# Performance work log

Measured on AMD Instinct MI355X. Metric: run time of the kernel, lower is better.

The kernel has to match this reference:

```python
import jax, jax.numpy as jnp
import numpy as np

B, R, L, E = 64, 36, 64, 512
LAMBDA_SOFTMAX = 9.0
NORM_EPS = 1e-12   # F.normalize eps
COS_EPS = 1e-8     # F.cosine_similarity eps


def _l2norm(x):
    return x / jnp.maximum(jnp.linalg.norm(x, axis=-1, keepdims=True), NORM_EPS)


def setup_inputs() -> dict:
    key = jax.random.key(0)
    k1, k2, k3 = jax.random.split(key, 3)
    images = jax.random.normal(k1, (B, R, E), dtype=jnp.float32)
    captions = jax.random.normal(k2, (B, L, E), dtype=jnp.float32)
    cap_lens = jax.random.randint(k3, (B,), 1, L + 1, dtype=jnp.int32)
    return {"images": images, "captions": captions, "cap_lens": cap_lens}


def reference(images, captions, cap_lens):
    # images: (B_img, R, E) region features; captions: (B_cap, L, E) token features
    img = _l2norm(images)
    cap = _l2norm(captions)

    # pairwise token-to-region similarity: (cap, img, L, R)
    sim = jnp.einsum('cle,ire->cilr', cap, img)
    # softmax over regions with temperature lambda_softmax.
    # NOTE: the original masks padded TOKEN rows with -inf before this softmax,
    # but those rows' outputs are fully zeroed below, so skipping the -inf fill
    # is mathematically equivalent (and NaN-free).
    attn_w = jax.nn.softmax(LAMBDA_SOFTMAX * sim, axis=-1)
    # attended image vector per (caption, image, token): (cap, img, L, E)
    attn = jnp.einsum('cilr,ire->cile', attn_w, img)

    # cosine similarity over feature dim
    dot = jnp.einsum('cle,cile->cil', cap, attn)
    na = jnp.linalg.norm(cap, axis=-1)[:, None, :]   # (cap, 1, L)
    nb = jnp.linalg.norm(attn, axis=-1)              # (cap, img, L)
    r = dot / jnp.maximum(na * nb, COS_EPS)          # (cap, img, L)

    # zero out padded tokens, then mean over the full padded length L
    valid = (jnp.arange(L)[None, :] < cap_lens[:, None]).astype(r.dtype)  # (cap, L)
    r = r * valid[:, None, :]
    sim_scores = r.mean(axis=-1)  # (cap, img)
    return sim_scores
```

## Files before the change

kernel.cpp:

```cpp
#include <hip/hip_runtime.h>
#include <stdint.h>

#define NCAP 64
#define NIMG 64
#define LTOK 64
#define RREG 36
#define EDIM 512
#define LAM 9.0f
#define SSTR 38

#define IMGT_STRIDE 18432

#define CHUNK_BYTES 34816
#define LDS_BYTES 77824

typedef __attribute__((ext_vector_type(8))) short bf16x8;
typedef __attribute__((ext_vector_type(4))) float f32x4;
typedef __attribute__((ext_vector_type(8))) unsigned short u16x8;

typedef const __attribute__((address_space(1))) void* gas1_t;
typedef __attribute__((address_space(3))) void* las3_t;

__device__ __forceinline__ void gl16(const void* g, void* l) {
  __builtin_amdgcn_global_load_lds((gas1_t)g, (las3_t)l, 16, 0, 0);
}

__device__ __forceinline__ unsigned short f2bf(float f) {
  unsigned int u = __float_as_uint(f);
  u += 0x7FFFu + ((u >> 16) & 1u);
  return (unsigned short)(u >> 16);
}

__global__ __launch_bounds__(256) void k_prep(const float* __restrict__ cap,
                                              const float* __restrict__ img,
                                              unsigned short* __restrict__ capT,
                                              unsigned short* __restrict__ imgT,
                                              float* __restrict__ G2) {
  __shared__ __align__(16) char gfr[49152];
  int tid = threadIdx.x;
  int w = tid >> 6, lane = tid & 63;
  int bid = blockIdx.x;

  if (bid < 64) {
    int i = bid;
    for (int t = tid; t < 1024; t += 256) {
      if ((t & 15) >= 4) {
        u16x8 z = {};
        *(u16x8*)(gfr + 32768 + t * 16) = z;
      }
    }
    int kk = lane >> 2, kg = lane & 3;
#pragma unroll
    for (int t = 0; t < 9; ++t) {
      int r = w + t * 4;
      const float* p = img + ((size_t)i * RREG + r) * EDIM + lane * 8;
      float4 a = *(const float4*)p;
      float4 b = *(const float4*)(p + 4);
      float ss = a.x * a.x + a.y * a.y + a.z * a.z + a.w * a.w +
                 b.x * b.x + b.y * b.y + b.z * b.z + b.w * b.w;
#pragma unroll
      for (int off = 1; off < 64; off <<= 1) ss += __shfl_xor(ss, off);
      float sc = 1.0f / fmaxf(sqrtf(ss), 1e-12f);
      u16x8 o = {f2bf(a.x * sc), f2bf(a.y * sc), f2bf(a.z * sc),
                 f2bf(a.w * sc), f2bf(b.x * sc), f2bf(b.y * sc),
                 f2bf(b.z * sc), f2bf(b.w * sc)};
      *(u16x8*)(gfr + (r >> 4) * 16384 + kk * 1024 +
                ((kg << 4) + (r & 15)) * 16) = o;
    }
    __syncthreads();
    if (w < 3) {
      f32x4 acc3[3];
#pragma unroll
      for (int n = 0; n < 3; ++n) acc3[n] = 0.f;
#pragma unroll
      for (int k2 = 0; k2 < 16; ++k2) {
        bf16x8 av = *(const bf16x8*)(gfr + w * 16384 + k2 * 1024 + lane * 16);
        bf16x8 b0 = *(const bf16x8*)(gfr + 0 * 16384 + k2 * 1024 + lane * 16);
        bf16x8 b1 = *(const bf16x8*)(gfr + 1 * 16384 + k2 * 1024 + lane * 16);
        bf16x8 b2 = *(const bf16x8*)(gfr + 2 * 16384 + k2 * 1024 + lane * 16);
        acc3[0] = __builtin_amdgcn_mfma_f32_16x16x32_bf16(av, b0, acc3[0], 0, 0, 0);
        acc3[1] = __builtin_amdgcn_mfma_f32_16x16x32_bf16(av, b1, acc3[1], 0, 0, 0);
        acc3[2] = __builtin_amdgcn_mfma_f32_16x16x32_bf16(av, b2, acc3[2], 0, 0, 0);
      }
      int rq = lane & 15, kgq = lane >> 4;
#pragma unroll
      for (int n = 0; n < 3; ++n)
#pragma unroll
        for (int j = 0; j < 4; ++j) {
          int R = w * 16 + kgq * 4 + j, C = n * 16 + rq;
          if (R < RREG && C < RREG) {
            float v = acc3[n][j];
            G2[(size_t)i * 1296 + R * 36 + C] = (R == C) ? v : 2.0f * v;
          }
        }
    }
    return;
  }

  int kkw = lane >> 2, kgw = lane & 3;
  int v = (bid - 64) * 4 + w;
  const float* p;
  unsigned short* dst;
  if (v < NCAP * LTOK) {
    int c = v >> 6, row = v & 63;
    int m = row >> 4, rqw = row & 15;
    p = cap + (size_t)v * EDIM + lane * 8;
    dst = capT + (size_t)c * 32768 +
          (size_t)(((m * 16 + kkw) * 64 + kgw * 16 + rqw) * 8);
  } else {
    int vi = v - NCAP * LTOK;
    int i = vi / RREG;
    int r = vi - i * RREG;
    p = img + ((size_t)i * RREG + r) * EDIM + lane * 8;
    if (r < 32) {
      int n = r >> 4, rqw = r & 15;
      dst = imgT + (size_t)i * IMGT_STRIDE +
            (size_t)(((n * 16 + kkw) * 64 + kgw * 16 + rqw) * 8);
    } else {
      int rq2 = r - 32;
      dst = imgT + (size_t)i * IMGT_STRIDE + 16384 +
            (size_t)(kkw * 128 + (kgw * 4 + rq2) * 8);
    }
  }
  float4 a = *(const float4*)p;
  float4 b = *(const float4*)(p + 4);
  float ss = a.x * a.x + a.y * a.y + a.z * a.z + a.w * a.w +
             b.x * b.x + b.y * b.y + b.z * b.z + b.w * b.w;
#pragma unroll
  for (int off = 1; off < 64; off <<= 1) ss += __shfl_xor(ss, off);
  float sc = 1.0f / fmaxf(sqrtf(ss), 1e-12f);
  u16x8 o = {f2bf(a.x * sc), f2bf(a.y * sc), f2bf(a.z * sc), f2bf(a.w * sc),
             f2bf(b.x * sc), f2bf(b.y * sc), f2bf(b.z * sc), f2bf(b.w * sc)};
  *(u16x8*)dst = o;
}

__device__ __forceinline__ void stage_chunk(const unsigned short* capT,
                                            const unsigned short* imgT,
                                            char* buf, int c0, int i0, int ch,
                                            int w, int lane) {
#pragma unroll
  for (int j = 0; j < 5; ++j) {
    int t = w + j * 8;
    if (t < 16) {
      int wcap = t >> 3, m = (t >> 1) & 3, kk = t & 1;
      const unsigned short* src =
          capT + (size_t)(c0 + wcap) * 32768 +
          (size_t)((m * 16 + ch * 2 + kk) * 512) + lane * 8;
      gl16(src, buf + (wcap * 8 + m * 2 + kk) * 1024);
    } else if (t < 32) {
      int u = t - 16;
      int kk = u >> 3, i = (u >> 1) & 3, f = u & 1;
      const unsigned short* src =
          imgT + (size_t)(i0 + i) * IMGT_STRIDE +
          (size_t)((f * 16 + ch * 2 + kk) * 512) + lane * 8;
      gl16(src, buf + 16384 + ((kk * 4 + i) * 2 + f) * 1024);
    } else if (t < 34) {
      int kk = t - 32;
      const unsigned short* src =
          imgT + (size_t)(i0 + (lane >> 4)) * IMGT_STRIDE + 16384 +
          (ch * 2 + kk) * 128 + (lane & 15) * 8;
      gl16(src, buf + 32768 + kk * 1024);
    }
  }
}

__global__ __launch_bounds__(512, 4) void k_main(
    const unsigned short* __restrict__ capT,
    const unsigned short* __restrict__ imgT, const float* __restrict__ G2,
    const int* __restrict__ lens, float* __restrict__ out) {
  __shared__ __align__(16) char lds[LDS_BYTES];
  int tid = threadIdx.x;
  int w = tid >> 6, lane = tid & 63;
  int wc = w >> 2, wi = w & 3;
  int rq = lane & 15, kg = lane >> 4;
  int bid = blockIdx.x;
  int b = (bid & 7) * 64 + (bid >> 3);
  int cg = b >> 4, ig = b & 15;
  int c0 = cg * 2, i0 = ig * 4;

  f32x4 acc[4][3];
#pragma unroll
  for (int m = 0; m < 4; ++m)
#pragma unroll
    for (int n = 0; n < 3; ++n) acc[m][n] = 0.f;

  stage_chunk(capT, imgT, lds, c0, i0, 0, w, lane);
#pragma unroll
  for (int ch = 0; ch < 8; ++ch) {
    char* cur = lds + (ch & 1) * CHUNK_BYTES;
    if (ch < 7) {
      stage_chunk(capT, imgT, lds + ((ch + 1) & 1) * CHUNK_BYTES, c0, i0,
                  ch + 1, w, lane);
      if (w < 2)
        asm volatile("s_waitcnt vmcnt(5)" ::: "memory");
      else
        asm volatile("s_waitcnt vmcnt(4)" ::: "memory");
    } else {
      asm volatile("s_waitcnt vmcnt(0)" ::: "memory");
    }
    __builtin_amdgcn_s_barrier();
    __builtin_amdgcn_sched_barrier(0);
    __builtin_amdgcn_s_setprio(1);
#pragma unroll
    for (int kk = 0; kk < 2; ++kk) {
      bf16x8 a0 = *(const bf16x8*)(cur + (wc * 8 + 0 * 2 + kk) * 1024 + lane * 16);
      bf16x8 a1 = *(const bf16x8*)(cur + (wc * 8 + 1 * 2 + kk) * 1024 + lane * 16);
      bf16x8 a2 = *(const bf16x8*)(cur + (wc * 8 + 2 * 2 + kk) * 1024 + lane * 16);
      bf16x8 a3 = *(const bf16x8*)(cur + (wc * 8 + 3 * 2 + kk) * 1024 + lane * 16);
      bf16x8 b0 = *(const bf16x8*)(cur + 16384 + ((kk * 4 + wi) * 2 + 0) * 1024 + lane * 16);
      bf16x8 b1 = *(const bf16x8*)(cur + 16384 + ((kk * 4 + wi) * 2 + 1) * 1024 + lane * 16);
      bf16x8 b2 = *(const bf16x8*)(cur + 32768 + kk * 1024 + wi * 256 +
                                   (kg * 4 + (rq & 3)) * 16);

      acc[0][0] = __builtin_amdgcn_mfma_f32_16x16x32_bf16(a0, b0, acc[0][0], 0, 0, 0);
      acc[0][1] = __builtin_amdgcn_mfma_f32_16x16x32_bf16(a0, b1, acc[0][1], 0, 0, 0);
      acc[0][2] = __builtin_amdgcn_mfma_f32_16x16x32_bf16(a0, b2, acc[0][2], 0, 0, 0);
      acc[1][0] = __builtin_amdgcn_mfma_f32_16x16x32_bf16(a1, b0, acc[1][0], 0, 0, 0);
      acc[1][1] = __builtin_amdgcn_mfma_f32_16x16x32_bf16(a1, b1, acc[1][1], 0, 0, 0);
      acc[1][2] = __builtin_amdgcn_mfma_f32_16x16x32_bf16(a1, b2, acc[1][2], 0, 0, 0);
      acc[2][0] = __builtin_amdgcn_mfma_f32_16x16x32_bf16(a2, b0, acc[2][0], 0, 0, 0);
      acc[2][1] = __builtin_amdgcn_mfma_f32_16x16x32_bf16(a2, b1, acc[2][1], 0, 0, 0);
      acc[2][2] = __builtin_amdgcn_mfma_f32_16x16x32_bf16(a2, b2, acc[2][2], 0, 0, 0);
      acc[3][0] = __builtin_amdgcn_mfma_f32_16x16x32_bf16(a3, b0, acc[3][0], 0, 0, 0);
      acc[3][1] = __builtin_amdgcn_mfma_f32_16x16x32_bf16(a3, b1, acc[3][1], 0, 0, 0);
      acc[3][2] = __builtin_amdgcn_mfma_f32_16x16x32_bf16(a3, b2, acc[3][2], 0, 0, 0);
    }
    __builtin_amdgcn_s_setprio(0);
    __builtin_amdgcn_sched_barrier(0);
    __builtin_amdgcn_s_barrier();
  }

  float* Sf = (float*)lds;
#pragma unroll
  for (int m = 0; m < 4; ++m)
#pragma unroll
    for (int n = 0; n < 3; ++n)
#pragma unroll
      for (int j = 0; j < 4; ++j)
        if (n < 2 || rq < 4)
          Sf[(w * 64 + m * 16 + kg * 4 + j) * SSTR + n * 16 + rq] =
              acc[m][n][j];
  __syncthreads();

  int c = c0 + (w >> 2);
  int i = i0 + (w & 3);
  const float* Srow = Sf + (size_t)(w * 64 + lane) * SSTR;
  float s[36];
#pragma unroll
  for (int r2 = 0; r2 < 18; ++r2) {
    float2 x = *(const float2*)(Srow + r2 * 2);
    s[r2 * 2 + 0] = x.x;
    s[r2 * 2 + 1] = x.y;
  }
  float mx = s[0];
#pragma unroll
  for (int r = 1; r < 36; ++r) mx = fmaxf(mx, s[r]);
  float p[36];
  float sum = 0.f, dotp = 0.f;
#pragma unroll
  for (int r = 0; r < 36; ++r) {
    p[r] = __expf(LAM * (s[r] - mx));
    sum += p[r];
    dotp = fmaf(p[r], s[r], dotp);
  }
  int iu = __builtin_amdgcn_readfirstlane(i);
  const float* Gi = G2 + (size_t)iu * 1296;
  float q2 = 0.f;
#pragma unroll
  for (int r2 = 0; r2 < 36; ++r2) {
    float t = 0.f;
#pragma unroll
    for (int r = 0; r <= r2; ++r) t = fmaf(Gi[r2 * 36 + r], p[r], t);
    q2 = fmaf(t, p[r2], q2);
  }
  float inv = 1.0f / sum;
  float dn = dotp * inv;
  float nb = sqrtf(fmaxf(q2, 0.f)) * inv;
  float rcos = dn / fmaxf(nb, 1e-8f);
  int len = lens[c];
  float val = (lane < len) ? rcos : 0.f;
#pragma unroll
  for (int off = 1; off < 64; off <<= 1) val += __shfl_xor(val, off);
  if (lane == 0) out[c * 64 + i] = val * (1.0f / 64.0f);
}

extern "C" void kernel_launch(void* const* d_in, const int* in_sizes, int n_in,
                              void* d_out, int out_size, void* d_ws,
                              size_t ws_size, hipStream_t stream) {
  const float* images = (const float*)d_in[0];
  const float* captions = (const float*)d_in[1];
  const int* lens = (const int*)d_in[2];
  float* out = (float*)d_out;

  char* ws = (char*)d_ws;
  unsigned short* capT = (unsigned short*)ws;
  unsigned short* imgT = (unsigned short*)(ws + 4194304);
  float* G = (float*)(ws + 4194304 + 2359296);

  k_prep<<<1664, 256, 0, stream>>>(captions, images, capT, imgT, G);
  k_main<<<512, 512, 0, stream>>>(capT, imgT, G, lens, out);
}
```

Before: 38.36 us.

## Single-buffer LDS and split softmax epilogue into two passes for higher occupancy

Halves the LDS footprint by dropping the double-buffered chunk pipeline for a single buffer with load, barrier, compute, barrier per chunk. The epilogue writes the score tile in two passes, one caption half per pass, so the tile fits in the smaller LDS. Launch bounds rise to 8 blocks per CU to hide latency with more resident workgroups. In exchange, global loads no longer overlap the MFMA work, there are extra barriers, and the higher occupancy target may force register spills given the large per-thread arrays.

```diff
diff --git a/kernel.cpp b/kernel.cpp
--- a/kernel.cpp
+++ b/kernel.cpp
@@ -12,7 +12,7 @@
 #define IMGT_STRIDE 18432
 
 #define CHUNK_BYTES 34816
-#define LDS_BYTES 77824
+#define LDS_BYTES 38912
 
 typedef __attribute__((ext_vector_type(8))) short bf16x8;
 typedef __attribute__((ext_vector_type(4))) float f32x4;
@@ -164,7 +164,7 @@
   }
 }
 
-__global__ __launch_bounds__(512, 4) void k_main(
+__global__ __launch_bounds__(512, 8) void k_main(
     const unsigned short* __restrict__ capT,
     const unsigned short* __restrict__ imgT, const float* __restrict__ G2,
     const int* __restrict__ lens, float* __restrict__ out) {
@@ -185,22 +185,10 @@
     for (int n = 0; n < 3; ++n) acc[m][n] = 0.f;
 
   stage_chunk(capT, imgT, lds, c0, i0, 0, w, lane);
+  __syncthreads();
 #pragma unroll
   for (int ch = 0; ch < 8; ++ch) {
-    char* cur = lds + (ch & 1) * CHUNK_BYTES;
-    if (ch < 7) {
-      stage_chunk(capT, imgT, lds + ((ch + 1) & 1) * CHUNK_BYTES, c0, i0,
-                  ch + 1, w, lane);
-      if (w < 2)
-        asm volatile("s_waitcnt vmcnt(5)" ::: "memory");
-      else
-        asm volatile("s_waitcnt vmcnt(4)" ::: "memory");
-    } else {
-      asm volatile("s_waitcnt vmcnt(0)" ::: "memory");
-    }
-    __builtin_amdgcn_s_barrier();
-    __builtin_amdgcn_sched_barrier(0);
-    __builtin_amdgcn_s_setprio(1);
+    char* cur = lds;
 #pragma unroll
     for (int kk = 0; kk < 2; ++kk) {
       bf16x8 a0 = *(const bf16x8*)(cur + (wc * 8 + 0 * 2 + kk) * 1024 + lane * 16);
@@ -225,63 +213,75 @@
       acc[3][1] = __builtin_amdgcn_mfma_f32_16x16x32_bf16(a3, b1, acc[3][1], 0, 0, 0);
       acc[3][2] = __builtin_amdgcn_mfma_f32_16x16x32_bf16(a3, b2, acc[3][2], 0, 0, 0);
     }
-    __builtin_amdgcn_s_setprio(0);
-    __builtin_amdgcn_sched_barrier(0);
-    __builtin_amdgcn_s_barrier();
+    __syncthreads();
+    if (ch < 7) {
+      stage_chunk(capT, imgT, lds, c0, i0, ch + 1, w, lane);
+      __syncthreads();
+    }
   }
 
   float* Sf = (float*)lds;
-#pragma unroll
-  for (int m = 0; m < 4; ++m)
-#pragma unroll
-    for (int n = 0; n < 3; ++n)
-#pragma unroll
-      for (int j = 0; j < 4; ++j)
-        if (n < 2 || rq < 4)
-          Sf[(w * 64 + m * 16 + kg * 4 + j) * SSTR + n * 16 + rq] =
-              acc[m][n][j];
-  __syncthreads();
-
-  int c = c0 + (w >> 2);
-  int i = i0 + (w & 3);
-  const float* Srow = Sf + (size_t)(w * 64 + lane) * SSTR;
-  float s[36];
-#pragma unroll
-  for (int r2 = 0; r2 < 18; ++r2) {
-    float2 x = *(const float2*)(Srow + r2 * 2);
-    s[r2 * 2 + 0] = x.x;
-    s[r2 * 2 + 1] = x.y;
-  }
-  float mx = s[0];
-#pragma unroll
-  for (int r = 1; r < 36; ++r) mx = fmaxf(mx, s[r]);
-  float p[36];
-  float sum = 0.f, dotp = 0.f;
-#pragma unroll
-  for (int r = 0; r < 36; ++r) {
-    p[r] = __expf(LAM * (s[r] - mx));
-    sum += p[r];
-    dotp = fmaf(p[r], s[r], dotp);
-  }
+  int c = c0 + wc;
+  int i = i0 + wi;
   int iu = __builtin_amdgcn_readfirstlane(i);
   const float* Gi = G2 + (size_t)iu * 1296;
-  float q2 = 0.f;
-#pragma unroll
-  for (int r2 = 0; r2 < 36; ++r2) {
-    float t = 0.f;
-#pragma unroll
-    for (int r = 0; r <= r2; ++r) t = fmaf(Gi[r2 * 36 + r], p[r], t);
-    q2 = fmaf(t, p[r2], q2);
-  }
-  float inv = 1.0f / sum;
-  float dn = dotp * inv;
-  float nb = sqrtf(fmaxf(q2, 0.f)) * inv;
-  float rcos = dn / fmaxf(nb, 1e-8f);
   int len = lens[c];
-  float val = (lane < len) ? rcos : 0.f;
-#pragma unroll
-  for (int off = 1; off < 64; off <<= 1) val += __shfl_xor(val, off);
-  if (lane == 0) out[c * 64 + i] = val * (1.0f / 64.0f);
+
+#pragma unroll
+  for (int pass = 0; pass < 2; ++pass) {
+    bool mine = (wc == pass);
+    int slot = wi;
+    if (mine) {
+#pragma unroll
+      for (int m = 0; m < 4; ++m)
+#pragma unroll
+        for (int n = 0; n < 3; ++n)
+#pragma unroll
+          for (int j = 0; j < 4; ++j)
+            if (n < 2 || rq < 4)
+              Sf[(slot * 64 + m * 16 + kg * 4 + j) * SSTR + n * 16 + rq] =
+                  acc[m][n][j];
+    }
+    __syncthreads();
+    if (mine) {
+      const float* Srow = Sf + (size_t)(slot * 64 + lane) * SSTR;
+      float s[36];
+#pragma unroll
+      for (int r2 = 0; r2 < 18; ++r2) {
+        float2 x = *(const float2*)(Srow + r2 * 2);
+        s[r2 * 2 + 0] = x.x;
+        s[r2 * 2 + 1] = x.y;
+      }
+      float mx = s[0];
+#pragma unroll
+      for (int r = 1; r < 36; ++r) mx = fmaxf(mx, s[r]);
+      float p[36];
+      float sum = 0.f, dotp = 0.f;
+#pragma unroll
+      for (int r = 0; r < 36; ++r) {
+        p[r] = __expf(LAM * (s[r] - mx));
+        sum += p[r];
+        dotp = fmaf(p[r], s[r], dotp);
+      }
+      float q2 = 0.f;
+#pragma unroll
+      for (int r2 = 0; r2 < 36; ++r2) {
+        float t = 0.f;
+#pragma unroll
+        for (int r = 0; r <= r2; ++r) t = fmaf(Gi[r2 * 36 + r], p[r], t);
+        q2 = fmaf(t, p[r2], q2);
+      }
+      float inv = 1.0f / sum;
+      float dn = dotp * inv;
+      float nb = sqrtf(fmaxf(q2, 0.f)) * inv;
+      float rcos = dn / fmaxf(nb, 1e-8f);
+      float val = (lane < len) ? rcos : 0.f;
+#pragma unroll
+      for (int off = 1; off < 64; off <<= 1) val += __shfl_xor(val, off);
+      if (lane == 0) out[c * 64 + i] = val * (1.0f / 64.0f);
+    }
+    if (pass == 0) __syncthreads();
+  }
 }
 
 extern "C" void kernel_launch(void* const* d_in, const int* in_sizes, int n_in,
```

Result: slower. 79.86 us (+108.2%).
